# Kernel optimization log

Hardware: AMD Instinct MI355X
Metric: run time of the kernel (lower is better)

Reference implementation:

```python
import jax, jax.numpy as jnp
import numpy as np

B, N, E = 32, 128, 16384
NI, NH, NO, NA = 72, 72, 72, 8
C_WEIGHT = 1.0
EPS = 1e-5  # torch BatchNorm1d default eps


def _psi(p):
    return jnp.sign(p) * jnp.log1p(jnp.abs(p))


def _normsq4(p):
    psq = p * p
    return 2.0 * psq[..., 0] - psq.sum(axis=-1)


def _dotsq4(p, q):
    psq = p * q
    return 2.0 * psq[..., 0] - psq.sum(axis=-1)


def _bn_train(z, g, b):
    # BatchNorm1d in training mode over flattened rows (biased variance)
    mu = z.mean(axis=0)
    var = z.var(axis=0)
    return (z - mu) * jax.lax.rsqrt(var + EPS) * g + b


def _seg_sum(data, ids):
    # data: [B,E,D], ids: [B,E] -> [B,N,D]
    return jax.vmap(lambda d, i: jax.ops.segment_sum(d, i, num_segments=N))(data, ids)


def _init(k, fan_in, shape, scale=1.0):
    return jax.random.normal(k, shape, jnp.float32) * (scale / np.sqrt(fan_in))


def setup_inputs() -> dict:
    key = jax.random.key(0)
    ks = jax.random.split(key, 24)
    d_e_in = 2 * NI + 2
    d_h_in = NH + NI + NA
    return {
        "h": jax.random.normal(ks[0], (B, N, NI), jnp.float32),
        "x": jax.random.normal(ks[1], (B, N, 4), jnp.float32),
        "edgei": jax.random.randint(ks[2], (B, E), 0, N, jnp.int32),
        "edgej": jax.random.randint(ks[3], (B, E), 0, N, jnp.int32),
        "node_attr": jax.random.normal(ks[4], (B, N, NA), jnp.float32),
        # phi_e: Linear(no bias) -> BN -> ReLU -> Linear -> ReLU
        "W_e1": _init(ks[5], d_e_in, (d_e_in, NH)),
        "g_e": jnp.ones((NH,), jnp.float32),
        "be_e": jnp.zeros((NH,), jnp.float32),
        "W_e2": _init(ks[6], NH, (NH, NH)),
        "b_e2": jnp.zeros((NH,), jnp.float32),
        # phi_m: Linear -> Sigmoid
        "W_m": _init(ks[7], NH, (NH, 1)),
        "b_m": jnp.zeros((1,), jnp.float32),
        # phi_x: Linear -> ReLU -> Linear(no bias, tiny xavier gain 0.001)
        "W_x1": _init(ks[8], NH, (NH, NH)),
        "b_x1": jnp.zeros((NH,), jnp.float32),
        "W_x2": _init(ks[9], NH, (NH, 1), scale=0.001),
        # phi_h: Linear -> BN -> ReLU -> Linear
        "W_h1": _init(ks[10], d_h_in, (d_h_in, NH)),
        "b_h1": jnp.zeros((NH,), jnp.float32),
        "g_h": jnp.ones((NH,), jnp.float32),
        "be_h": jnp.zeros((NH,), jnp.float32),
        "W_h2": _init(ks[11], NH, (NH, NO)),
        "b_h2": jnp.zeros((NO,), jnp.float32),
    }


def reference(h, x, edgei, edgej, node_attr, W_e1, g_e, be_e, W_e2, b_e2,
              W_m, b_m, W_x1, b_x1, W_x2, W_h1, b_h1, g_h, be_h, W_h2, b_h2):
    ii = edgei[..., None]  # [B,E,1]
    jj = edgej[..., None]
    # minkowski_feats
    xi = jnp.take_along_axis(x, ii, axis=1)  # [B,E,4]
    xj = jnp.take_along_axis(x, jj, axis=1)
    x_diff = xi - xj
    norms = _psi(_normsq4(x_diff))[..., None]  # [B,E,1]
    dots = _psi(_dotsq4(xi, xj))[..., None]
    # m_model
    hi = jnp.take_along_axis(h, ii, axis=1)  # [B,E,NI]
    hj = jnp.take_along_axis(h, jj, axis=1)
    feat = jnp.concatenate([hi, hj, norms, dots], axis=-1).reshape(-1, 2 * NI + 2)
    z = jax.nn.relu(_bn_train(feat @ W_e1, g_e, be_e))
    z = jax.nn.relu(z @ W_e2 + b_e2)
    m_e = z.reshape(B, E, NH)
    w = jax.nn.sigmoid(m_e @ W_m + b_m)  # [B,E,1]
    m = m_e * w
    # x_model (not last_layer)
    phix = jax.nn.relu(m @ W_x1 + b_x1) @ W_x2  # [B,E,1]
    trans = jnp.clip(x_diff * phix, -100.0, 100.0)
    agg = _seg_sum(trans, edgei)
    cnt = _seg_sum(jnp.ones_like(trans), edgei)
    x_out = x + (agg / jnp.maximum(cnt, 1.0)) * C_WEIGHT
    # h_model
    magg = _seg_sum(m, edgei)  # [B,N,NH]
    cat = jnp.concatenate([h, magg, node_attr], axis=-1).reshape(-1, NH + NI + NA)
    zh = jax.nn.relu(_bn_train(cat @ W_h1 + b_h1, g_h, be_h))
    zh = zh @ W_h2 + b_h2
    h_out = h + zh.reshape(B, N, NO)
    return (h_out, x_out, m)
```

## Files before the change

### kernel.cpp

```cpp
#include <hip/hip_runtime.h>
#include <math.h>

#define B_ 32
#define N_ 128
#define E_ 16384
#define EPS_ 1e-5f

typedef short short8v __attribute__((ext_vector_type(8)));
typedef float f32x4v __attribute__((ext_vector_type(4)));

#define FADD(p, v) unsafeAtomicAdd((p), (v))

#define WS_MAGG    4608
#define WS_AGG     299520
#define WS_CNT     315904
#define WS_ZERO_END 320000
#define WS_AE      320000
#define WS_BE      320072
#define WS_AH      320144
#define WS_BH      320216
#define WS_ZH1     325472
#define WS_PERM    325472
#define WS_HIST    587616
#define WS_OFFS    591712
#define WS_CURS    595808

#define HOUT_OFF 0
#define XOUT_OFF 294912
#define M_OFF    311296

#define NSTAT_T 147456
#define MSTR 88

static __device__ __forceinline__ short f2bf(float f) {
    unsigned int u = __builtin_bit_cast(unsigned int, f);
    u += 0x7FFFu + ((u >> 16) & 1u);
    return (short)(u >> 16);
}

__global__ __launch_bounds__(256) void k_nodeproj(
    const float* __restrict__ h, const float* __restrict__ We1,
    float* __restrict__ Ptop, float* __restrict__ Pmid)
{
    int blk = blockIdx.x;
    int rowBlk = blk >> 3, sub = blk & 7;
    int which = sub >> 2, q = sub & 3;
    int row = rowBlk * 256 + threadIdx.x;
    int c0 = q * 18;
    const float4* h4 = (const float4*)(h + (size_t)row * 72);
    const float* base = We1 + which * 5184 + c0;
    float acc[18];
#pragma unroll
    for (int c = 0; c < 18; ++c) acc[c] = 0.f;
    for (int kc = 0; kc < 18; ++kc) {
        float4 a = h4[kc];
        const float* wr = base + (kc * 4) * 72;
#pragma unroll
        for (int c = 0; c < 18; ++c)
            acc[c] = fmaf(a.x, wr[c], fmaf(a.y, wr[72 + c], fmaf(a.z, wr[144 + c], fmaf(a.w, wr[216 + c], acc[c]))));
    }
    float* P = (which ? Pmid : Ptop) + (size_t)row * 72 + c0;
#pragma unroll
    for (int c = 0; c < 18; ++c) P[c] = acc[c];
}

__global__ __launch_bounds__(256) void k_edge1v3(
    const float* __restrict__ x,
    const int* __restrict__ ei, const int* __restrict__ ej,
    const float* __restrict__ Ptop, const float* __restrict__ Pmid,
    const float* __restrict__ We1,
    float* __restrict__ z1)
{
    int eg = blockIdx.x * 256 + threadIdx.x;
    int b = eg >> 14;
    int i = ei[eg], j = ej[eg];
    int ri = b * N_ + i, rj = b * N_ + j;

    float4 xi = *(const float4*)(x + ri * 4);
    float4 xj = *(const float4*)(x + rj * 4);
    float xdx = xi.x - xj.x, xdy = xi.y - xj.y, xdz = xi.z - xj.z, xdw = xi.w - xj.w;
    float nsq = xdx * xdx - xdy * xdy - xdz * xdz - xdw * xdw;
    float dsq = xi.x * xj.x - xi.y * xj.y - xi.z * xj.z - xi.w * xj.w;
    float norms = copysignf(log1pf(fabsf(nsq)), nsq);
    float dots  = copysignf(log1pf(fabsf(dsq)), dsq);

    const float4* pt4 = (const float4*)(Ptop + (size_t)ri * 72);
    const float4* pm4 = (const float4*)(Pmid + (size_t)rj * 72);
    const float* w144 = We1 + 144 * 72;
    const float* w145 = We1 + 145 * 72;
    float4* zr = (float4*)(z1 + (size_t)eg * 72);

#pragma unroll
    for (int kc = 0; kc < 18; ++kc) {
        float4 a = pt4[kc];
        float4 bq = pm4[kc];
        float4 wa = *(const float4*)(w144 + 4 * kc);
        float4 wb = *(const float4*)(w145 + 4 * kc);
        float4 r;
        r.x = fmaf(norms, wa.x, fmaf(dots, wb.x, a.x + bq.x));
        r.y = fmaf(norms, wa.y, fmaf(dots, wb.y, a.y + bq.y));
        r.z = fmaf(norms, wa.z, fmaf(dots, wb.z, a.z + bq.z));
        r.w = fmaf(norms, wa.w, fmaf(dots, wb.w, a.w + bq.w));
        zr[kc] = r;
    }
}

__global__ __launch_bounds__(256) void k_hist(
    const int* __restrict__ ei, int* __restrict__ hist)
{
    __shared__ int lh[128];
    int t = threadIdx.x;
    if (t < 128) lh[t] = 0;
    __syncthreads();
    int eg = blockIdx.x * 256 + t;
    int b = eg >> 14;
    atomicAdd(&lh[ei[eg]], 1);
    __syncthreads();
    if (t < 128) {
        int v = lh[t];
        if (v) atomicAdd(&hist[b * N_ + t], v);
    }
}

__global__ void k_scan(const int* __restrict__ hist, int* __restrict__ offs,
                       int* __restrict__ curs, float* __restrict__ cnt)
{
    __shared__ int sh[128];
    int b = blockIdx.x, n = threadIdx.x;
    int cv = hist[b * N_ + n];
    sh[n] = cv;
    __syncthreads();
    for (int off = 1; off < 128; off <<= 1) {
        int v = (n >= off) ? sh[n - off] : 0;
        __syncthreads();
        sh[n] += v;
        __syncthreads();
    }
    int excl = sh[n] - cv;
    offs[b * N_ + n] = excl;
    curs[b * N_ + n] = excl;
    cnt[b * N_ + n] = (float)cv;
}

__global__ __launch_bounds__(256) void k_scatter(
    const int* __restrict__ ei, int* __restrict__ curs,
    unsigned short* __restrict__ perm)
{
    int eg = blockIdx.x * 256 + threadIdx.x;
    int b = eg >> 14;
    int i = ei[eg];
    int pos = atomicAdd(&curs[b * N_ + i], 1);
    perm[(size_t)b * E_ + pos] = (unsigned short)(eg & (E_ - 1));
}

__global__ __launch_bounds__(256) void k_stats(
    const float* __restrict__ src, float* __restrict__ sPart,
    float* __restrict__ qPart, int iters)
{
    int tid = blockIdx.x * 256 + threadIdx.x;
    float s0 = 0.f, s1 = 0.f, s2 = 0.f, s3 = 0.f;
    float q0 = 0.f, q1 = 0.f, q2 = 0.f, q3 = 0.f;
    size_t idx = tid;
    const size_t st = NSTAT_T;
    int it = 0;
    for (; it + 3 < iters; it += 4, idx += 4 * st) {
        float v0 = src[idx];
        float v1 = src[idx + st];
        float v2 = src[idx + 2 * st];
        float v3 = src[idx + 3 * st];
        s0 += v0; q0 = fmaf(v0, v0, q0);
        s1 += v1; q1 = fmaf(v1, v1, q1);
        s2 += v2; q2 = fmaf(v2, v2, q2);
        s3 += v3; q3 = fmaf(v3, v3, q3);
    }
    for (; it < iters; ++it, idx += st) {
        float v = src[idx];
        s0 += v; q0 = fmaf(v, v, q0);
    }
    sPart[tid] = (s0 + s1) + (s2 + s3);
    qPart[tid] = (q0 + q1) + (q2 + q3);
}

__global__ __launch_bounds__(256) void k_red(
    const float* __restrict__ sPart, const float* __restrict__ qPart,
    float* __restrict__ sRed, float* __restrict__ qRed)
{
    int tid = blockIdx.x * 256 + threadIdx.x;
    if (tid >= 4608) return;
    int g = tid / 72, c = tid - g * 72;
    int k0 = g * 32;
    float s0 = 0.f, s1 = 0.f, q0 = 0.f, q1 = 0.f;
#pragma unroll 4
    for (int k = 0; k < 32; k += 2) {
        s0 += sPart[c + 72 * (k0 + k)];
        s1 += sPart[c + 72 * (k0 + k + 1)];
        q0 += qPart[c + 72 * (k0 + k)];
        q1 += qPart[c + 72 * (k0 + k + 1)];
    }
    sRed[c + 72 * g] = s0 + s1;
    qRed[c + 72 * g] = q0 + q1;
}

__global__ void k_fin2c(const float* __restrict__ sRed, const float* __restrict__ qRed,
                        const float* __restrict__ g, const float* __restrict__ be,
                        float* __restrict__ A, float* __restrict__ Bv, float Minv)
{
    __shared__ float ss[288], qs[288];
    int t = threadIdx.x;
    int c = t % 72, qq = t / 72;
    float s = 0.f, q = 0.f;
    for (int k = qq; k < 64; k += 4) {
        s += sRed[c + 72 * k];
        q += qRed[c + 72 * k];
    }
    ss[t] = s; qs[t] = q;
    __syncthreads();
    if (t < 72) {
        s = ss[t] + ss[t + 72] + ss[t + 144] + ss[t + 216];
        q = qs[t] + qs[t + 72] + qs[t + 144] + qs[t + 216];
        float mu = s * Minv;
        float var = q * Minv - mu * mu;
        float inv = rsqrtf(var + EPS_);
        float a = g[t] * inv;
        A[t] = a;
        Bv[t] = be[t] - mu * a;
    }
}

__global__ __launch_bounds__(256) void k_e2f(
    const float* __restrict__ x,
    const int* __restrict__ ei, const int* __restrict__ ej,
    const float* __restrict__ We2, const float* __restrict__ be2,
    const float* __restrict__ Wm, const float* __restrict__ bm,
    const float* __restrict__ bx1, const float* __restrict__ Wx1,
    const float* __restrict__ Wx2,
    const float* __restrict__ Ae, const float* __restrict__ Be,
    float* mz, float* __restrict__ agg)
{
    __shared__ short W2S[80 * 104];
    __shared__ short WxS[80 * 104];
    __shared__ short mS[4][16 * MSTR];
    __shared__ float lagg[128 * 5];
    int t = threadIdx.x;
    for (int idx = t; idx < 128 * 5; idx += 256) lagg[idx] = 0.f;
    for (int idx = t; idx < 80 * 104; idx += 256) {
        int n = idx / 104, k = idx - n * 104;
        bool v = (n < 72 && k < 72);
        W2S[idx] = f2bf(v ? We2[k * 72 + n] : 0.f);
        WxS[idx] = f2bf(v ? Wx1[k * 72 + n] : 0.f);
    }
    __syncthreads();

    int base = blockIdx.x * 256;
    int b = base >> 14;
    int w = t >> 6, l = t & 63, ln = l & 15, g4 = l >> 4;
    float bm0 = bm[0];

    float4 a00 = *(const float4*)(Ae + g4 * 8),      a01 = *(const float4*)(Ae + g4 * 8 + 4);
    float4 b00 = *(const float4*)(Be + g4 * 8),      b01 = *(const float4*)(Be + g4 * 8 + 4);
    float4 a10 = *(const float4*)(Ae + 32 + g4 * 8), a11 = *(const float4*)(Ae + 32 + g4 * 8 + 4);
    float4 b10 = *(const float4*)(Be + 32 + g4 * 8), b11 = *(const float4*)(Be + 32 + g4 * 8 + 4);
    float4 a20, a21, b20, b21;
    if (g4 == 0) {
        a20 = *(const float4*)(Ae + 64); a21 = *(const float4*)(Ae + 68);
        b20 = *(const float4*)(Be + 64); b21 = *(const float4*)(Be + 68);
    } else {
        a20 = make_float4(0, 0, 0, 0); a21 = a20; b20 = a20; b21 = a20;
    }
    float be2v[5], wmv[5], bxv[5], wxv[5];
#pragma unroll
    for (int nt = 0; nt < 5; ++nt) {
        int chan = nt * 16 + ln;
        bool cv = chan < 72;
        be2v[nt] = cv ? be2[chan] : 0.f;
        wmv[nt]  = cv ? Wm[chan]  : 0.f;
        bxv[nt]  = cv ? bx1[chan] : 0.f;
        wxv[nt]  = cv ? Wx2[chan] : 0.f;
    }
    const short8v zero8 = {0, 0, 0, 0, 0, 0, 0, 0};
    {
#pragma unroll
        for (int q = 0; q < 4; ++q)
            mS[w][(l & 15) * MSTR + 72 + ((l >> 4) & 3) * 4 + q] = 0;
    }

    for (int ts = 0; ts < 4; ++ts) {
        int es = base + w * 64 + ts * 16;
        const float* zrow = mz + (size_t)(es + ln) * 72 + g4 * 8;
        float4 c0a = *(const float4*)(zrow);
        float4 c0b = *(const float4*)(zrow + 4);
        float4 c1a = *(const float4*)(zrow + 32);
        float4 c1b = *(const float4*)(zrow + 36);

        short8v az0, az1, az2 = zero8;
        az0[0] = f2bf(fmaxf(fmaf(c0a.x, a00.x, b00.x), 0.f));
        az0[1] = f2bf(fmaxf(fmaf(c0a.y, a00.y, b00.y), 0.f));
        az0[2] = f2bf(fmaxf(fmaf(c0a.z, a00.z, b00.z), 0.f));
        az0[3] = f2bf(fmaxf(fmaf(c0a.w, a00.w, b00.w), 0.f));
        az0[4] = f2bf(fmaxf(fmaf(c0b.x, a01.x, b01.x), 0.f));
        az0[5] = f2bf(fmaxf(fmaf(c0b.y, a01.y, b01.y), 0.f));
        az0[6] = f2bf(fmaxf(fmaf(c0b.z, a01.z, b01.z), 0.f));
        az0[7] = f2bf(fmaxf(fmaf(c0b.w, a01.w, b01.w), 0.f));
        az1[0] = f2bf(fmaxf(fmaf(c1a.x, a10.x, b10.x), 0.f));
        az1[1] = f2bf(fmaxf(fmaf(c1a.y, a10.y, b10.y), 0.f));
        az1[2] = f2bf(fmaxf(fmaf(c1a.z, a10.z, b10.z), 0.f));
        az1[3] = f2bf(fmaxf(fmaf(c1a.w, a10.w, b10.w), 0.f));
        az1[4] = f2bf(fmaxf(fmaf(c1b.x, a11.x, b11.x), 0.f));
        az1[5] = f2bf(fmaxf(fmaf(c1b.y, a11.y, b11.y), 0.f));
        az1[6] = f2bf(fmaxf(fmaf(c1b.z, a11.z, b11.z), 0.f));
        az1[7] = f2bf(fmaxf(fmaf(c1b.w, a11.w, b11.w), 0.f));
        if (g4 == 0) {
            float4 c2a = *(const float4*)(mz + (size_t)(es + ln) * 72 + 64);
            float4 c2b = *(const float4*)(mz + (size_t)(es + ln) * 72 + 68);
            az2[0] = f2bf(fmaxf(fmaf(c2a.x, a20.x, b20.x), 0.f));
            az2[1] = f2bf(fmaxf(fmaf(c2a.y, a20.y, b20.y), 0.f));
            az2[2] = f2bf(fmaxf(fmaf(c2a.z, a20.z, b20.z), 0.f));
            az2[3] = f2bf(fmaxf(fmaf(c2a.w, a20.w, b20.w), 0.f));
            az2[4] = f2bf(fmaxf(fmaf(c2b.x, a21.x, b21.x), 0.f));
            az2[5] = f2bf(fmaxf(fmaf(c2b.y, a21.y, b21.y), 0.f));
            az2[6] = f2bf(fmaxf(fmaf(c2b.z, a21.z, b21.z), 0.f));
            az2[7] = f2bf(fmaxf(fmaf(c2b.w, a21.w, b21.w), 0.f));
        }

        f32x4v acc[5];
#pragma unroll
        for (int nt = 0; nt < 5; ++nt) { f32x4v zz = {0.f, 0.f, 0.f, 0.f}; acc[nt] = zz; }
#pragma unroll
        for (int nt = 0; nt < 5; ++nt) {
            int rb = (nt * 16 + ln) * 104 + g4 * 8;
            short8v bw0 = *(const short8v*)&W2S[rb];
            short8v bw1 = *(const short8v*)&W2S[rb + 32];
            short8v bw2 = *(const short8v*)&W2S[rb + 64];
            acc[nt] = __builtin_amdgcn_mfma_f32_16x16x32_bf16(az0, bw0, acc[nt], 0, 0, 0);
            acc[nt] = __builtin_amdgcn_mfma_f32_16x16x32_bf16(az1, bw1, acc[nt], 0, 0, 0);
            acc[nt] = __builtin_amdgcn_mfma_f32_16x16x32_bf16(az2, bw2, acc[nt], 0, 0, 0);
        }

        float mt[5][4];
        float wdot[4] = {bm0, bm0, bm0, bm0};
#pragma unroll
        for (int nt = 0; nt < 5; ++nt) {
#pragma unroll
            for (int r = 0; r < 4; ++r) {
                mt[nt][r] = fmaxf(acc[nt][r] + be2v[nt], 0.f);
                wdot[r] = fmaf(mt[nt][r], wmv[nt], wdot[r]);
            }
        }
#pragma unroll
        for (int r = 0; r < 4; ++r) {
            wdot[r] += __shfl_xor(wdot[r], 1);
            wdot[r] += __shfl_xor(wdot[r], 2);
            wdot[r] += __shfl_xor(wdot[r], 4);
            wdot[r] += __shfl_xor(wdot[r], 8);
            wdot[r] = 1.f / (1.f + expf(-wdot[r]));
        }
#pragma unroll
        for (int nt = 0; nt < 5; ++nt) {
            int chan = nt * 16 + ln;
#pragma unroll
            for (int r = 0; r < 4; ++r) {
                float mv = mt[nt][r] * wdot[r];
                mS[w][(g4 * 4 + r) * MSTR + chan] = f2bf(mv);
                if (chan < 72)
                    mz[(size_t)(es + g4 * 4 + r) * 72 + chan] = mv;
            }
        }
        __syncthreads();

        short8v am0 = *(const short8v*)&mS[w][ln * MSTR + g4 * 8];
        short8v am1 = *(const short8v*)&mS[w][ln * MSTR + 32 + g4 * 8];
        short8v am2 = zero8;
        if (g4 == 0) am2 = *(const short8v*)&mS[w][ln * MSTR + 64];

        f32x4v acc3[5];
#pragma unroll
        for (int nt = 0; nt < 5; ++nt) { f32x4v zz = {0.f, 0.f, 0.f, 0.f}; acc3[nt] = zz; }
#pragma unroll
        for (int nt = 0; nt < 5; ++nt) {
            int rb = (nt * 16 + ln) * 104 + g4 * 8;
            short8v bw0 = *(const short8v*)&WxS[rb];
            short8v bw1 = *(const short8v*)&WxS[rb + 32];
            short8v bw2 = *(const short8v*)&WxS[rb + 64];
            acc3[nt] = __builtin_amdgcn_mfma_f32_16x16x32_bf16(am0, bw0, acc3[nt], 0, 0, 0);
            acc3[nt] = __builtin_amdgcn_mfma_f32_16x16x32_bf16(am1, bw1, acc3[nt], 0, 0, 0);
            acc3[nt] = __builtin_amdgcn_mfma_f32_16x16x32_bf16(am2, bw2, acc3[nt], 0, 0, 0);
        }

        float ph[4] = {0.f, 0.f, 0.f, 0.f};
#pragma unroll
        for (int nt = 0; nt < 5; ++nt) {
#pragma unroll
            for (int r = 0; r < 4; ++r)
                ph[r] = fmaf(fmaxf(acc3[nt][r] + bxv[nt], 0.f), wxv[nt], ph[r]);
        }
#pragma unroll
        for (int r = 0; r < 4; ++r) {
            ph[r] += __shfl_xor(ph[r], 1);
            ph[r] += __shfl_xor(ph[r], 2);
            ph[r] += __shfl_xor(ph[r], 4);
            ph[r] += __shfl_xor(ph[r], 8);
        }
        if (ln == 0) {
#pragma unroll
            for (int r = 0; r < 4; ++r) {
                int eg = es + g4 * 4 + r;
                int ii = ei[eg], jj = ej[eg];
                float4 xi = *(const float4*)(x + (size_t)(b * N_ + ii) * 4);
                float4 xj = *(const float4*)(x + (size_t)(b * N_ + jj) * 4);
                float phx = ph[r];
                float trx = fminf(fmaxf((xi.x - xj.x) * phx, -100.f), 100.f);
                float try_ = fminf(fmaxf((xi.y - xj.y) * phx, -100.f), 100.f);
                float trz = fminf(fmaxf((xi.z - xj.z) * phx, -100.f), 100.f);
                float trw = fminf(fmaxf((xi.w - xj.w) * phx, -100.f), 100.f);
                FADD(&lagg[ii * 5 + 0], trx);
                FADD(&lagg[ii * 5 + 1], try_);
                FADD(&lagg[ii * 5 + 2], trz);
                FADD(&lagg[ii * 5 + 3], trw);
            }
        }
        __syncthreads();
    }

    int nb = b * N_;
    for (int idx = t; idx < 128 * 4; idx += 256) {
        int n = idx >> 2, d = idx & 3;
        float v = lagg[n * 5 + d];
        if (v != 0.f) FADD(&agg[(nb + n) * 4 + d], v);
    }
}

__global__ __launch_bounds__(256) void k_seg2(
    const float* __restrict__ m, const unsigned short* __restrict__ perm,
    const int* __restrict__ offs, const int* __restrict__ hist,
    float* __restrict__ magg)
{
    int tid = blockIdx.x * 256 + threadIdx.x;
    int g = tid / 72, c = tid - g * 72;
    int b = g >> 7;
    int start = offs[g];
    int count = hist[g];
    const unsigned short* p = perm + (size_t)b * E_ + start;
    const float* mb = m + (size_t)b * E_ * 72 + c;
    float a0 = 0.f, a1 = 0.f;
    int k = 0;
    for (; k + 1 < count; k += 2) {
        int e0 = p[k], e1 = p[k + 1];
        a0 += mb[(size_t)e0 * 72];
        a1 += mb[(size_t)e1 * 72];
    }
    if (k < count) a0 += mb[(size_t)p[k] * 72];
    magg[(size_t)g * 72 + c] = a0 + a1;
}

__global__ __launch_bounds__(256) void k_node1v3(
    const float* __restrict__ h, const float* __restrict__ magg,
    const float* __restrict__ attr, const float* __restrict__ Wh1,
    const float* __restrict__ bh1, float* __restrict__ zh1)
{
    int blk = blockIdx.x;
    int q = blk >> 4;
    int row = (blk & 15) * 256 + threadIdx.x;
    int c0 = q * 9;
    float acc[9];
#pragma unroll
    for (int c = 0; c < 9; ++c) acc[c] = bh1[c0 + c];

    const float4* h4 = (const float4*)(h + (size_t)row * 72);
    for (int kc = 0; kc < 18; ++kc) {
        float4 a = h4[kc];
        const float* wr = Wh1 + (kc * 4) * 72 + c0;
#pragma unroll
        for (int c = 0; c < 9; ++c)
            acc[c] = fmaf(a.x, wr[c], fmaf(a.y, wr[72 + c], fmaf(a.z, wr[144 + c], fmaf(a.w, wr[216 + c], acc[c]))));
    }
    const float4* mg4 = (const float4*)(magg + (size_t)row * 72);
    for (int kc = 0; kc < 18; ++kc) {
        float4 a = mg4[kc];
        const float* wr = Wh1 + (72 + kc * 4) * 72 + c0;
#pragma unroll
        for (int c = 0; c < 9; ++c)
            acc[c] = fmaf(a.x, wr[c], fmaf(a.y, wr[72 + c], fmaf(a.z, wr[144 + c], fmaf(a.w, wr[216 + c], acc[c]))));
    }
    const float4* at4 = (const float4*)(attr + (size_t)row * 8);
    for (int kc = 0; kc < 2; ++kc) {
        float4 a = at4[kc];
        const float* wr = Wh1 + (144 + kc * 4) * 72 + c0;
#pragma unroll
        for (int c = 0; c < 9; ++c)
            acc[c] = fmaf(a.x, wr[c], fmaf(a.y, wr[72 + c], fmaf(a.z, wr[144 + c], fmaf(a.w, wr[216 + c], acc[c]))));
    }
    float* zr = zh1 + (size_t)row * 72 + c0;
#pragma unroll
    for (int c = 0; c < 9; ++c) zr[c] = acc[c];
}

__global__ __launch_bounds__(256) void k_node2v2(
    const float* __restrict__ h, const float* __restrict__ x,
    const float* __restrict__ zh1,
    const float* __restrict__ Ah, const float* __restrict__ Bh,
    const float* __restrict__ Wh2, const float* __restrict__ bh2,
    const float* __restrict__ agg, const float* __restrict__ cnt,
    float* __restrict__ hout, float* __restrict__ xout)
{
    int blk = blockIdx.x;
    int q = blk >> 4;
    int row = (blk & 15) * 256 + threadIdx.x;
    int c0 = q * 9;
    float acc[9];
#pragma unroll
    for (int c = 0; c < 9; ++c) acc[c] = bh2[c0 + c];

    const float4* z4 = (const float4*)(zh1 + (size_t)row * 72);
    for (int kc = 0; kc < 18; ++kc) {
        float4 v = z4[kc];
        int k0 = kc * 4;
        float z0 = fmaxf(fmaf(v.x, Ah[k0],     Bh[k0]),     0.f);
        float z1v = fmaxf(fmaf(v.y, Ah[k0 + 1], Bh[k0 + 1]), 0.f);
        float z2v = fmaxf(fmaf(v.z, Ah[k0 + 2], Bh[k0 + 2]), 0.f);
        float z3v = fmaxf(fmaf(v.w, Ah[k0 + 3], Bh[k0 + 3]), 0.f);
        const float* w0 = Wh2 + k0 * 72 + c0;
#pragma unroll
        for (int c = 0; c < 9; ++c)
            acc[c] = fmaf(z0, w0[c], fmaf(z1v, w0[72 + c], fmaf(z2v, w0[144 + c], fmaf(z3v, w0[216 + c], acc[c]))));
    }
    const float* hr = h + (size_t)row * 72 + c0;
    float* ho = hout + (size_t)row * 72 + c0;
#pragma unroll
    for (int c = 0; c < 9; ++c) ho[c] = hr[c] + acc[c];

    if (q == 0) {
        float inv = 1.f / fmaxf(cnt[row], 1.f);
        float4 xv = *(const float4*)(x + (size_t)row * 4);
        float4 av = *(const float4*)(agg + (size_t)row * 4);
        *(float4*)(xout + (size_t)row * 4) = make_float4(xv.x + av.x * inv, xv.y + av.y * inv,
                                                         xv.z + av.z * inv, xv.w + av.w * inv);
    }
}

extern "C" void kernel_launch(void* const* d_in, const int* in_sizes, int n_in,
                              void* d_out, int out_size, void* d_ws, size_t ws_size,
                              hipStream_t stream) {
    const float* h    = (const float*)d_in[0];
    const float* x    = (const float*)d_in[1];
    const int*   ei   = (const int*)d_in[2];
    const int*   ej   = (const int*)d_in[3];
    const float* attr = (const float*)d_in[4];
    const float* We1  = (const float*)d_in[5];
    const float* ge   = (const float*)d_in[6];
    const float* bee  = (const float*)d_in[7];
    const float* We2  = (const float*)d_in[8];
    const float* be2  = (const float*)d_in[9];
    const float* Wm   = (const float*)d_in[10];
    const float* bm   = (const float*)d_in[11];
    const float* Wx1  = (const float*)d_in[12];
    const float* bx1  = (const float*)d_in[13];
    const float* Wx2  = (const float*)d_in[14];
    const float* Wh1  = (const float*)d_in[15];
    const float* bh1  = (const float*)d_in[16];
    const float* gh   = (const float*)d_in[17];
    const float* beh  = (const float*)d_in[18];
    const float* Wh2  = (const float*)d_in[19];
    const float* bh2  = (const float*)d_in[20];

    float* out  = (float*)d_out;
    float* hout = out + HOUT_OFF;
    float* xout = out + XOUT_OFF;
    float* mz   = out + M_OFF;
    float* ws   = (float*)d_ws;
    float* sRed = xout;
    float* qRed = xout + 4608;

    hipMemsetAsync(ws, 0, (size_t)WS_ZERO_END * 4, stream);
    k_nodeproj<<<128, 256, 0, stream>>>(h, We1, ws + WS_ZH1, ws + WS_MAGG);
    k_edge1v3<<<2048, 256, 0, stream>>>(x, ei, ej, ws + WS_ZH1, ws + WS_MAGG, We1, mz);
    hipMemsetAsync(ws + WS_HIST, 0, 4096 * 4, stream);
    k_hist<<<2048, 256, 0, stream>>>(ei, (int*)(ws + WS_HIST));
    k_scan<<<32, 128, 0, stream>>>((const int*)(ws + WS_HIST), (int*)(ws + WS_OFFS),
                                   (int*)(ws + WS_CURS), ws + WS_CNT);
    k_scatter<<<2048, 256, 0, stream>>>(ei, (int*)(ws + WS_CURS),
                                        (unsigned short*)(ws + WS_PERM));
    k_stats<<<576, 256, 0, stream>>>(mz, ws + WS_MAGG, ws + WS_MAGG + NSTAT_T, 256);
    k_red<<<18, 256, 0, stream>>>(ws + WS_MAGG, ws + WS_MAGG + NSTAT_T, sRed, qRed);
    k_fin2c<<<1, 288, 0, stream>>>(sRed, qRed, ge, bee,
                                   ws + WS_AE, ws + WS_BE, 1.0f / (float)(B_ * E_));
    k_e2f<<<2048, 256, 0, stream>>>(x, ei, ej, We2, be2, Wm, bm, bx1, Wx1, Wx2,
                                    ws + WS_AE, ws + WS_BE, mz, ws + WS_AGG);
    k_seg2<<<1152, 256, 0, stream>>>(mz, (const unsigned short*)(ws + WS_PERM),
                                     (const int*)(ws + WS_OFFS), (const int*)(ws + WS_HIST),
                                     ws + WS_MAGG);
    k_node1v3<<<128, 256, 0, stream>>>(h, ws + WS_MAGG, attr, Wh1, bh1, ws + WS_ZH1);
    k_stats<<<576, 256, 0, stream>>>(ws + WS_ZH1, hout, hout + NSTAT_T, 2);
    k_red<<<18, 256, 0, stream>>>(hout, hout + NSTAT_T, sRed, qRed);
    k_fin2c<<<1, 288, 0, stream>>>(sRed, qRed, gh, beh,
                                   ws + WS_AH, ws + WS_BH, 1.0f / 4096.0f);
    k_node2v2<<<128, 256, 0, stream>>>(h, x, ws + WS_ZH1, ws + WS_AH, ws + WS_BH, Wh2, bh2,
                                       ws + WS_AGG, ws + WS_CNT, hout, xout);
}
```

Before: 363.3 us.

## Store pre-BN edge activations as bf16 and fuse histogram into edge kernel

```diff
diff --git a/kernel.cpp b/kernel.cpp
--- a/kernel.cpp
+++ b/kernel.cpp
@@ -19,9 +19,9 @@
 #define WS_BE      320072
 #define WS_AH      320144
 #define WS_BH      320216
+#define WS_HIST    320288
 #define WS_ZH1     325472
 #define WS_PERM    325472
-#define WS_HIST    587616
 #define WS_OFFS    591712
 #define WS_CURS    595808
 
@@ -36,6 +36,18 @@
     unsigned int u = __builtin_bit_cast(unsigned int, f);
     u += 0x7FFFu + ((u >> 16) & 1u);
     return (short)(u >> 16);
+}
+static __device__ __forceinline__ unsigned int pack2(float a, float b) {
+    return (unsigned int)(unsigned short)f2bf(a) | ((unsigned int)(unsigned short)f2bf(b) << 16);
+}
+static __device__ __forceinline__ float b2f(unsigned short u) {
+    return __builtin_bit_cast(float, (unsigned int)u << 16);
+}
+static __device__ __forceinline__ float b2f_lo(unsigned int u) {
+    return __builtin_bit_cast(float, u << 16);
+}
+static __device__ __forceinline__ float b2f_hi(unsigned int u) {
+    return __builtin_bit_cast(float, u & 0xFFFF0000u);
 }
 
 __global__ __launch_bounds__(256) void k_nodeproj(
@@ -64,16 +76,22 @@
     for (int c = 0; c < 18; ++c) P[c] = acc[c];
 }
 
-__global__ __launch_bounds__(256) void k_edge1v3(
+__global__ __launch_bounds__(256) void k_edge1v4(
     const float* __restrict__ x,
     const int* __restrict__ ei, const int* __restrict__ ej,
     const float* __restrict__ Ptop, const float* __restrict__ Pmid,
     const float* __restrict__ We1,
-    float* __restrict__ z1)
-{
-    int eg = blockIdx.x * 256 + threadIdx.x;
+    unsigned short* __restrict__ zG, int* __restrict__ hist)
+{
+    __shared__ int lh[128];
+    int t = threadIdx.x;
+    if (t < 128) lh[t] = 0;
+    __syncthreads();
+
+    int eg = blockIdx.x * 256 + t;
     int b = eg >> 14;
     int i = ei[eg], j = ej[eg];
+    atomicAdd(&lh[i], 1);
     int ri = b * N_ + i, rj = b * N_ + j;
 
     float4 xi = *(const float4*)(x + ri * 4);
@@ -88,33 +106,29 @@
     const float4* pm4 = (const float4*)(Pmid + (size_t)rj * 72);
     const float* w144 = We1 + 144 * 72;
     const float* w145 = We1 + 145 * 72;
-    float4* zr = (float4*)(z1 + (size_t)eg * 72);
-
-#pragma unroll
-    for (int kc = 0; kc < 18; ++kc) {
-        float4 a = pt4[kc];
-        float4 bq = pm4[kc];
-        float4 wa = *(const float4*)(w144 + 4 * kc);
-        float4 wb = *(const float4*)(w145 + 4 * kc);
-        float4 r;
-        r.x = fmaf(norms, wa.x, fmaf(dots, wb.x, a.x + bq.x));
-        r.y = fmaf(norms, wa.y, fmaf(dots, wb.y, a.y + bq.y));
-        r.z = fmaf(norms, wa.z, fmaf(dots, wb.z, a.z + bq.z));
-        r.w = fmaf(norms, wa.w, fmaf(dots, wb.w, a.w + bq.w));
-        zr[kc] = r;
-    }
-}
-
-__global__ __launch_bounds__(256) void k_hist(
-    const int* __restrict__ ei, int* __restrict__ hist)
-{
-    __shared__ int lh[128];
-    int t = threadIdx.x;
-    if (t < 128) lh[t] = 0;
-    __syncthreads();
-    int eg = blockIdx.x * 256 + t;
-    int b = eg >> 14;
-    atomicAdd(&lh[ei[eg]], 1);
+    uint4* zr = (uint4*)(zG + (size_t)eg * 144);
+
+#pragma unroll
+    for (int g = 0; g < 9; ++g) {
+        float4 a0 = pt4[2 * g],     bq0 = pm4[2 * g];
+        float4 a1 = pt4[2 * g + 1], bq1 = pm4[2 * g + 1];
+        float4 wa0 = *(const float4*)(w144 + 8 * g);
+        float4 wb0 = *(const float4*)(w145 + 8 * g);
+        float4 wa1 = *(const float4*)(w144 + 8 * g + 4);
+        float4 wb1 = *(const float4*)(w145 + 8 * g + 4);
+        float r0 = fmaf(norms, wa0.x, fmaf(dots, wb0.x, a0.x + bq0.x));
+        float r1 = fmaf(norms, wa0.y, fmaf(dots, wb0.y, a0.y + bq0.y));
+        float r2 = fmaf(norms, wa0.z, fmaf(dots, wb0.z, a0.z + bq0.z));
+        float r3 = fmaf(norms, wa0.w, fmaf(dots, wb0.w, a0.w + bq0.w));
+        float r4 = fmaf(norms, wa1.x, fmaf(dots, wb1.x, a1.x + bq1.x));
+        float r5 = fmaf(norms, wa1.y, fmaf(dots, wb1.y, a1.y + bq1.y));
+        float r6 = fmaf(norms, wa1.z, fmaf(dots, wb1.z, a1.z + bq1.z));
+        float r7 = fmaf(norms, wa1.w, fmaf(dots, wb1.w, a1.w + bq1.w));
+        uint4 u;
+        u.x = pack2(r0, r1); u.y = pack2(r2, r3);
+        u.z = pack2(r4, r5); u.w = pack2(r6, r7);
+        zr[g] = u;
+    }
     __syncthreads();
     if (t < 128) {
         int v = lh[t];
@@ -153,32 +167,43 @@
     perm[(size_t)b * E_ + pos] = (unsigned short)(eg & (E_ - 1));
 }
 
-__global__ __launch_bounds__(256) void k_stats(
-    const float* __restrict__ src, float* __restrict__ sPart,
-    float* __restrict__ qPart, int iters)
+__global__ __launch_bounds__(256) void k_stats_bf(
+    const unsigned short* __restrict__ zG,
+    float* __restrict__ sPart, float* __restrict__ qPart)
 {
     int tid = blockIdx.x * 256 + threadIdx.x;
+    int c = tid % 72, e0 = tid / 72;
     float s0 = 0.f, s1 = 0.f, s2 = 0.f, s3 = 0.f;
     float q0 = 0.f, q1 = 0.f, q2 = 0.f, q3 = 0.f;
-    size_t idx = tid;
-    const size_t st = NSTAT_T;
-    int it = 0;
-    for (; it + 3 < iters; it += 4, idx += 4 * st) {
-        float v0 = src[idx];
-        float v1 = src[idx + st];
-        float v2 = src[idx + 2 * st];
-        float v3 = src[idx + 3 * st];
+    size_t idx = (size_t)e0 * 144 + c;
+    const size_t step = (size_t)2048 * 144;
+    for (int k = 0; k < 256; k += 4, idx += 4 * step) {
+        float v0 = b2f(zG[idx]);
+        float v1 = b2f(zG[idx + step]);
+        float v2 = b2f(zG[idx + 2 * step]);
+        float v3 = b2f(zG[idx + 3 * step]);
         s0 += v0; q0 = fmaf(v0, v0, q0);
         s1 += v1; q1 = fmaf(v1, v1, q1);
         s2 += v2; q2 = fmaf(v2, v2, q2);
         s3 += v3; q3 = fmaf(v3, v3, q3);
     }
-    for (; it < iters; ++it, idx += st) {
+    sPart[tid] = (s0 + s1) + (s2 + s3);
+    qPart[tid] = (q0 + q1) + (q2 + q3);
+}
+
+__global__ __launch_bounds__(256) void k_stats(
+    const float* __restrict__ src, float* __restrict__ sPart,
+    float* __restrict__ qPart, int iters)
+{
+    int tid = blockIdx.x * 256 + threadIdx.x;
+    float s0 = 0.f, q0 = 0.f;
+    size_t idx = tid;
+    for (int it = 0; it < iters; ++it, idx += NSTAT_T) {
         float v = src[idx];
         s0 += v; q0 = fmaf(v, v, q0);
     }
-    sPart[tid] = (s0 + s1) + (s2 + s3);
-    qPart[tid] = (q0 + q1) + (q2 + q3);
+    sPart[tid] = s0;
+    qPart[tid] = q0;
 }
 
 __global__ __launch_bounds__(256) void k_red(
@@ -235,7 +260,7 @@
     const float* __restrict__ bx1, const float* __restrict__ Wx1,
     const float* __restrict__ Wx2,
     const float* __restrict__ Ae, const float* __restrict__ Be,
-    float* mz, float* __restrict__ agg)
+    const unsigned short* zG, float* mz, float* __restrict__ agg)
 {
     __shared__ short W2S[80 * 104];
     __shared__ short WxS[80 * 104];
@@ -286,40 +311,37 @@
 
     for (int ts = 0; ts < 4; ++ts) {
         int es = base + w * 64 + ts * 16;
-        const float* zrow = mz + (size_t)(es + ln) * 72 + g4 * 8;
-        float4 c0a = *(const float4*)(zrow);
-        float4 c0b = *(const float4*)(zrow + 4);
-        float4 c1a = *(const float4*)(zrow + 32);
-        float4 c1b = *(const float4*)(zrow + 36);
+        const unsigned short* zrow = zG + (size_t)(es + ln) * 144;
+        uint4 u0 = *(const uint4*)(zrow + g4 * 8);
+        uint4 u1 = *(const uint4*)(zrow + 32 + g4 * 8);
 
         short8v az0, az1, az2 = zero8;
-        az0[0] = f2bf(fmaxf(fmaf(c0a.x, a00.x, b00.x), 0.f));
-        az0[1] = f2bf(fmaxf(fmaf(c0a.y, a00.y, b00.y), 0.f));
-        az0[2] = f2bf(fmaxf(fmaf(c0a.z, a00.z, b00.z), 0.f));
-        az0[3] = f2bf(fmaxf(fmaf(c0a.w, a00.w, b00.w), 0.f));
-        az0[4] = f2bf(fmaxf(fmaf(c0b.x, a01.x, b01.x), 0.f));
-        az0[5] = f2bf(fmaxf(fmaf(c0b.y, a01.y, b01.y), 0.f));
-        az0[6] = f2bf(fmaxf(fmaf(c0b.z, a01.z, b01.z), 0.f));
-        az0[7] = f2bf(fmaxf(fmaf(c0b.w, a01.w, b01.w), 0.f));
-        az1[0] = f2bf(fmaxf(fmaf(c1a.x, a10.x, b10.x), 0.f));
-        az1[1] = f2bf(fmaxf(fmaf(c1a.y, a10.y, b10.y), 0.f));
-        az1[2] = f2bf(fmaxf(fmaf(c1a.z, a10.z, b10.z), 0.f));
-        az1[3] = f2bf(fmaxf(fmaf(c1a.w, a10.w, b10.w), 0.f));
-        az1[4] = f2bf(fmaxf(fmaf(c1b.x, a11.x, b11.x), 0.f));
-        az1[5] = f2bf(fmaxf(fmaf(c1b.y, a11.y, b11.y), 0.f));
-        az1[6] = f2bf(fmaxf(fmaf(c1b.z, a11.z, b11.z), 0.f));
-        az1[7] = f2bf(fmaxf(fmaf(c1b.w, a11.w, b11.w), 0.f));
+        az0[0] = f2bf(fmaxf(fmaf(b2f_lo(u0.x), a00.x, b00.x), 0.f));
+        az0[1] = f2bf(fmaxf(fmaf(b2f_hi(u0.x), a00.y, b00.y), 0.f));
+        az0[2] = f2bf(fmaxf(fmaf(b2f_lo(u0.y), a00.z, b00.z), 0.f));
+        az0[3] = f2bf(fmaxf(fmaf(b2f_hi(u0.y), a00.w, b00.w), 0.f));
+        az0[4] = f2bf(fmaxf(fmaf(b2f_lo(u0.z), a01.x, b01.x), 0.f));
+        az0[5] = f2bf(fmaxf(fmaf(b2f_hi(u0.z), a01.y, b01.y), 0.f));
+        az0[6] = f2bf(fmaxf(fmaf(b2f_lo(u0.w), a01.z, b01.z), 0.f));
+        az0[7] = f2bf(fmaxf(fmaf(b2f_hi(u0.w), a01.w, b01.w), 0.f));
+        az1[0] = f2bf(fmaxf(fmaf(b2f_lo(u1.x), a10.x, b10.x), 0.f));
+        az1[1] = f2bf(fmaxf(fmaf(b2f_hi(u1.x), a10.y, b10.y), 0.f));
+        az1[2] = f2bf(fmaxf(fmaf(b2f_lo(u1.y), a10.z, b10.z), 0.f));
+        az1[3] = f2bf(fmaxf(fmaf(b2f_hi(u1.y), a10.w, b10.w), 0.f));
+        az1[4] = f2bf(fmaxf(fmaf(b2f_lo(u1.z), a11.x, b11.x), 0.f));
+        az1[5] = f2bf(fmaxf(fmaf(b2f_hi(u1.z), a11.y, b11.y), 0.f));
+        az1[6] = f2bf(fmaxf(fmaf(b2f_lo(u1.w), a11.z, b11.z), 0.f));
+        az1[7] = f2bf(fmaxf(fmaf(b2f_hi(u1.w), a11.w, b11.w), 0.f));
         if (g4 == 0) {
-            float4 c2a = *(const float4*)(mz + (size_t)(es + ln) * 72 + 64);
-            float4 c2b = *(const float4*)(mz + (size_t)(es + ln) * 72 + 68);
-            az2[0] = f2bf(fmaxf(fmaf(c2a.x, a20.x, b20.x), 0.f));
-            az2[1] = f2bf(fmaxf(fmaf(c2a.y, a20.y, b20.y), 0.f));
-            az2[2] = f2bf(fmaxf(fmaf(c2a.z, a20.z, b20.z), 0.f));
-            az2[3] = f2bf(fmaxf(fmaf(c2a.w, a20.w, b20.w), 0.f));
-            az2[4] = f2bf(fmaxf(fmaf(c2b.x, a21.x, b21.x), 0.f));
-            az2[5] = f2bf(fmaxf(fmaf(c2b.y, a21.y, b21.y), 0.f));
-            az2[6] = f2bf(fmaxf(fmaf(c2b.z, a21.z, b21.z), 0.f));
-            az2[7] = f2bf(fmaxf(fmaf(c2b.w, a21.w, b21.w), 0.f));
+            uint4 u2 = *(const uint4*)(zrow + 64);
+            az2[0] = f2bf(fmaxf(fmaf(b2f_lo(u2.x), a20.x, b20.x), 0.f));
+            az2[1] = f2bf(fmaxf(fmaf(b2f_hi(u2.x), a20.y, b20.y), 0.f));
+            az2[2] = f2bf(fmaxf(fmaf(b2f_lo(u2.y), a20.z, b20.z), 0.f));
+            az2[3] = f2bf(fmaxf(fmaf(b2f_hi(u2.y), a20.w, b20.w), 0.f));
+            az2[4] = f2bf(fmaxf(fmaf(b2f_lo(u2.z), a21.x, b21.x), 0.f));
+            az2[5] = f2bf(fmaxf(fmaf(b2f_hi(u2.z), a21.y, b21.y), 0.f));
+            az2[6] = f2bf(fmaxf(fmaf(b2f_lo(u2.w), a21.z, b21.z), 0.f));
+            az2[7] = f2bf(fmaxf(fmaf(b2f_hi(u2.w), a21.w, b21.w), 0.f));
         }
 
         f32x4v acc[5];
@@ -566,25 +588,26 @@
     float* hout = out + HOUT_OFF;
     float* xout = out + XOUT_OFF;
     float* mz   = out + M_OFF;
+    unsigned short* zG = (unsigned short*)mz;
     float* ws   = (float*)d_ws;
     float* sRed = xout;
     float* qRed = xout + 4608;
 
     hipMemsetAsync(ws, 0, (size_t)WS_ZERO_END * 4, stream);
+    hipMemsetAsync(ws + WS_HIST, 0, 4096 * 4, stream);
     k_nodeproj<<<128, 256, 0, stream>>>(h, We1, ws + WS_ZH1, ws + WS_MAGG);
-    k_edge1v3<<<2048, 256, 0, stream>>>(x, ei, ej, ws + WS_ZH1, ws + WS_MAGG, We1, mz);
-    hipMemsetAsync(ws + WS_HIST, 0, 4096 * 4, stream);
-    k_hist<<<2048, 256, 0, stream>>>(ei, (int*)(ws + WS_HIST));
+    k_edge1v4<<<2048, 256, 0, stream>>>(x, ei, ej, ws + WS_ZH1, ws + WS_MAGG, We1,
+                                        zG, (int*)(ws + WS_HIST));
     k_scan<<<32, 128, 0, stream>>>((const int*)(ws + WS_HIST), (int*)(ws + WS_OFFS),
                                    (int*)(ws + WS_CURS), ws + WS_CNT);
     k_scatter<<<2048, 256, 0, stream>>>(ei, (int*)(ws + WS_CURS),
                                         (unsigned short*)(ws + WS_PERM));
-    k_stats<<<576, 256, 0, stream>>>(mz, ws + WS_MAGG, ws + WS_MAGG + NSTAT_T, 256);
+    k_stats_bf<<<576, 256, 0, stream>>>(zG, ws + WS_MAGG, ws + WS_MAGG + NSTAT_T);
     k_red<<<18, 256, 0, stream>>>(ws + WS_MAGG, ws + WS_MAGG + NSTAT_T, sRed, qRed);
     k_fin2c<<<1, 288, 0, stream>>>(sRed, qRed, ge, bee,
                                    ws + WS_AE, ws + WS_BE, 1.0f / (float)(B_ * E_));
     k_e2f<<<2048, 256, 0, stream>>>(x, ei, ej, We2, be2, Wm, bm, bx1, Wx1, Wx2,
-                                    ws + WS_AE, ws + WS_BE, mz, ws + WS_AGG);
+                                    ws + WS_AE, ws + WS_BE, zG, mz, ws + WS_AGG);
     k_seg2<<<1152, 256, 0, stream>>>(mz, (const unsigned short*)(ws + WS_PERM),
                                      (const int*)(ws + WS_OFFS), (const int*)(ws + WS_HIST),
                                      ws + WS_MAGG);
```

After: 329.0 us (median of 2 runs). 1.1x faster.
